# Kernel tuning notes

Hardware: AMD Instinct MI355X
Metric: run time of the kernel (lower is better)

## Reference

```python
import jax, jax.numpy as jnp
import numpy as np

SEQ_LEN, PRED_LEN, ENC_IN, BS = 512, 512, 64, 64


def _main_freq_part(x, k):
    # x: [b, L, c]; rfft over time axis, keep top-k magnitude freqs per (b, c)
    xf = jnp.fft.rfft(x, axis=1)                       # [b, F, c] complex
    mag = jnp.abs(xf)
    _, idx = jax.lax.top_k(jnp.moveaxis(mag, 1, 2), k)  # [b, c, k]
    F = xf.shape[1]
    mask = jax.nn.one_hot(idx, F, dtype=x.dtype).sum(axis=2)  # [b, c, F]
    mask = jnp.moveaxis(mask, 1, 2)                    # [b, F, c]
    x_filt = jnp.fft.irfft(xf * mask, axis=1).astype(jnp.float32)  # n = 2*(F-1) = L (L even)
    return x - x_filt, x_filt


def setup_inputs() -> dict:
    key = jax.random.key(0)
    ks = jax.random.split(key, 16)
    E = ENC_IN
    s = 0.05
    inp = {
        "batch_x": jax.random.normal(ks[0], (BS, SEQ_LEN, ENC_IN), dtype=jnp.float32),
        # nn.MultiheadAttention params (num_heads resolves to 1)
        "in_proj_w": jax.random.normal(ks[1], (3 * E, E), dtype=jnp.float32) * s,
        "in_proj_b": jax.random.normal(ks[2], (3 * E,), dtype=jnp.float32) * s,
        "out_w": jax.random.normal(ks[3], (E, E), dtype=jnp.float32) * s,
        "out_b": jax.random.normal(ks[4], (E,), dtype=jnp.float32) * s,
        # FANLayer params
        "Wp": jax.random.normal(ks[5], (PRED_LEN // 4, SEQ_LEN), dtype=jnp.float32) * s,
        "bp": jax.random.normal(ks[6], (PRED_LEN // 4,), dtype=jnp.float32) * s,
        "Wg": jax.random.normal(ks[7], (PRED_LEN - PRED_LEN // 2, SEQ_LEN), dtype=jnp.float32) * s,
        "bg": jax.random.normal(ks[8], (PRED_LEN - PRED_LEN // 2,), dtype=jnp.float32) * s,
        "gate": jax.random.normal(ks[9], (1,), dtype=jnp.float32),
        # MLP params (input_dim = seq_len + pred_len)
        "fc1_w": jax.random.normal(ks[10], (3 * (SEQ_LEN + PRED_LEN), SEQ_LEN + PRED_LEN), dtype=jnp.float32) * s,
        "fc1_b": jax.random.normal(ks[11], (3 * (SEQ_LEN + PRED_LEN),), dtype=jnp.float32) * s,
        "fc2_w": jax.random.normal(ks[12], (PRED_LEN, 3 * (SEQ_LEN + PRED_LEN)), dtype=jnp.float32) * s,
        "fc2_b": jax.random.normal(ks[13], (PRED_LEN,), dtype=jnp.float32) * s,
        "freq_topk": 20,
    }
    return inp


def reference(batch_x, in_proj_w, in_proj_b, out_w, out_b,
              Wp, bp, Wg, bg, gate, fc1_w, fc1_b, fc2_w, fc2_b, freq_topk):
    E = batch_x.shape[-1]
    norm_input, x_filt = _main_freq_part(batch_x, freq_topk)  # [b, L, c] each

    # --- single-head MultiheadAttention: Q = x_filt, K = V = norm_input ---
    wq, wk, wv = jnp.split(in_proj_w, 3, axis=0)
    bq, bk, bv = jnp.split(in_proj_b, 3, axis=0)
    q = x_filt @ wq.T + bq
    k = norm_input @ wk.T + bk
    v = norm_input @ wv.T + bv
    scores = jnp.einsum('bqe,bke->bqk', q, k) / jnp.sqrt(jnp.asarray(E, batch_x.dtype))
    attn = jax.nn.softmax(scores, axis=-1)
    attn_output = jnp.einsum('bqk,bke->bqe', attn, v) @ out_w.T + out_b  # [b, L, c]

    # --- FANLayer (identical weights per channel -> fully batched) ---
    mf = jnp.swapaxes(x_filt, 1, 2)     # [b, c, L]
    xt = jnp.swapaxes(batch_x, 1, 2)    # [b, c, L]
    g = jax.nn.gelu(mf @ Wg.T + bg, approximate=False)
    p = mf @ Wp.T + bp
    gt = jax.nn.sigmoid(gate)           # (1,) broadcasts
    fan = jnp.concatenate([gt * jnp.cos(p), gt * jnp.sin(p), (1.0 - gt) * g], axis=-1)  # [b, c, pred]
    h = jnp.concatenate([fan, xt], axis=-1)          # [b, c, L + pred]
    mlp = jax.nn.relu(h @ fc1_w.T + fc1_b) @ fc2_w.T + fc2_b  # [b, c, pred]
    pred_main = jnp.swapaxes(mlp, 1, 2)              # [b, pred, c]

    # torch forward('n') returns attn_output and stores pred_main as state;
    # stack both to expose all computed math.
    return jnp.stack([attn_output, pred_main])
```

## Files before the change

kernel.cpp:

```cpp
#include <hip/hip_runtime.h>
#include <math.h>

#define U_HBF   0
#define U_MFT   4194304
#define U_XRE   6291456
#define U_XIM   7344128
#define U_KEEPI 8396800
#define U_KEEPW 8527872
#define U_XFILT 8658944
#define U_NORM  10756096
#define U_Q     6291456
#define U_K     12853248
#define U_V     14950400
#define U_HIDBF 8388608
#define U_W1BF  14680064
#define U_W2BF  16252928
#define U_PART  8658944

#define TWO_PI_OVER_512 0.012271846303085129

typedef __attribute__((ext_vector_type(8))) short short8;
typedef __attribute__((ext_vector_type(4))) float floatx4;

__device__ inline unsigned short f2bf(float f) {
    union { unsigned int i; float f; } x; x.f = f;
    unsigned int r = x.i + 0x7fff + ((x.i >> 16) & 1);
    return (unsigned short)(r >> 16);
}

__global__ __launch_bounds__(256) void dft_split(const float* __restrict__ x,
                                                 float* __restrict__ xre,
                                                 float* __restrict__ xim,
                                                 float* __restrict__ part) {
    __shared__ float xs[64 * 64];
    __shared__ float ct[512], st[512];
    int tid = threadIdx.x;
    int b = blockIdx.y;
    int f0 = blockIdx.x * 64;
    int z = blockIdx.z;
    for (int i = tid; i < 512; i += 256) {
        float s, c; sincosf((float)((double)i * TWO_PI_OVER_512), &s, &c);
        ct[i] = c; st[i] = s;
    }
    int c2 = (tid & 31) * 2;
    int fg = tid >> 5;
    int fb = f0 + fg * 8;
    float2 ar[8], ai[8];
    #pragma unroll
    for (int i = 0; i < 8; ++i) { ar[i] = make_float2(0.f, 0.f); ai[i] = make_float2(0.f, 0.f); }
    for (int sub = 0; sub < 2; ++sub) {
        int t0 = z * 128 + sub * 64;
        __syncthreads();
        for (int i = tid; i < 4096; i += 256)
            xs[i] = x[(size_t)(b * 512 + t0) * 64 + i];
        __syncthreads();
        for (int tt = 0; tt < 64; ++tt) {
            float2 xv = *(float2*)&xs[tt * 64 + c2];
            int t = t0 + tt;
            int idx = (fb * t) & 511;
            #pragma unroll
            for (int i = 0; i < 8; ++i) {
                float cv = ct[idx], sv = st[idx];
                ar[i].x += xv.x * cv; ar[i].y += xv.y * cv;
                ai[i].x -= xv.x * sv; ai[i].y -= xv.y * sv;
                idx = (idx + t) & 511;
            }
        }
    }
    float* dre = (z == 0) ? xre : (part + (size_t)(z - 1) * 2105344);
    float* dim_ = (z == 0) ? xim : (part + (size_t)(z - 1) * 2105344 + 1052672);
    #pragma unroll
    for (int i = 0; i < 8; ++i) {
        int f = fb + i;
        if (f < 257) {
            *(float2*)&dre[((size_t)(b * 257) + f) * 64 + c2] = ar[i];
            *(float2*)&dim_[((size_t)(b * 257) + f) * 64 + c2] = ai[i];
        }
    }
}

__global__ __launch_bounds__(256) void dft_reduce(float* __restrict__ xreflat,
                                                  const float* __restrict__ part) {
    int i = blockIdx.x * 256 + threadIdx.x;
    if (i < 526336) {
        float4 a  = *(float4*)&xreflat[(size_t)i * 4];
        float4 p0 = *(const float4*)&part[(size_t)i * 4];
        float4 p1 = *(const float4*)&part[2105344 + (size_t)i * 4];
        float4 p2 = *(const float4*)&part[4210688 + (size_t)i * 4];
        a.x += p0.x + p1.x + p2.x;
        a.y += p0.y + p1.y + p2.y;
        a.z += p0.z + p1.z + p2.z;
        a.w += p0.w + p1.w + p2.w;
        *(float4*)&xreflat[(size_t)i * 4] = a;
    }
}

__global__ __launch_bounds__(256) void topk_lds(const float* __restrict__ xre,
                                                const float* __restrict__ xim,
                                                int* __restrict__ keepi,
                                                float* __restrict__ keepw,
                                                const int* __restrict__ kptr) {
    __shared__ float vals[320];
    __shared__ float tv[256];
    __shared__ int   ti[256];
    int tid = threadIdx.x;
    int bc = blockIdx.x;
    int b = bc >> 6, c = bc & 63;
    int kk = *kptr; if (kk > 32) kk = 32;
    for (int f = tid; f < 320; f += 256) {
        if (f < 257) {
            size_t a = ((size_t)(b * 257) + f) * 64 + c;
            float re = xre[a], im = xim[a];
            vals[f] = sqrtf(re * re + im * im);
        } else vals[f] = -1.f;
    }
    __syncthreads();
    for (int j = 0; j < kk; ++j) {
        float v0 = vals[tid];
        int   i0 = tid;
        if (tid < 64) {
            float v1 = vals[tid + 256];
            if (v1 > v0) { v0 = v1; i0 = tid + 256; }
        }
        tv[tid] = v0; ti[tid] = i0;
        __syncthreads();
        for (int s = 128; s > 0; s >>= 1) {
            if (tid < s) {
                float ov = tv[tid + s]; int oi = ti[tid + s];
                if (ov > tv[tid] || (ov == tv[tid] && oi < ti[tid])) { tv[tid] = ov; ti[tid] = oi; }
            }
            __syncthreads();
        }
        if (tid == 0) {
            int bf = ti[0];
            keepi[bc * 32 + j] = bf;
            keepw[bc * 32 + j] = (bf == 0 || bf == 256) ? (1.f / 512.f) : (2.f / 512.f);
            vals[bf] = -1.f;
        }
        __syncthreads();
    }
}

__global__ __launch_bounds__(256) void xfilt_fused(const float* __restrict__ x,
                                                   const float* __restrict__ xre,
                                                   const float* __restrict__ xim,
                                                   const int* __restrict__ keepi,
                                                   const float* __restrict__ keepw,
                                                   float* __restrict__ xfilt,
                                                   float* __restrict__ norm,
                                                   float* __restrict__ mft,
                                                   unsigned short* __restrict__ hbf,
                                                   const int* __restrict__ kptr) {
    __shared__ float ct[512], st[512];
    __shared__ int   kf[64 * 33];
    __shared__ float kre[64 * 33], kim[64 * 33];
    __shared__ float xs[64 * 65];
    __shared__ float ft[64 * 65];
    int tid = threadIdx.x;
    int b = blockIdx.y;
    int t0 = blockIdx.x * 64;
    int kk = *kptr; if (kk > 32) kk = 32;
    for (int i = tid; i < 512; i += 256) {
        float s, c; sincosf((float)((double)i * TWO_PI_OVER_512), &s, &c);
        ct[i] = c; st[i] = s;
    }
    for (int i = tid; i < 4096; i += 256) {
        int tl = i >> 6, c = i & 63;
        xs[tl * 65 + c] = x[((size_t)(b * 512) + t0 + tl) * 64 + c];
    }
    for (int e = tid; e < 64 * kk; e += 256) {
        int c = e / kk, j = e - c * kk;
        int bc = b * 64 + c;
        int f = keepi[bc * 32 + j];
        float w = keepw[bc * 32 + j];
        size_t a = ((size_t)(b * 257) + f) * 64 + c;
        kf[c * 33 + j]  = f;
        kre[c * 33 + j] = w * xre[a];
        kim[c * 33 + j] = w * xim[a];
    }
    __syncthreads();
    int l = tid & 63, w = tid >> 6;
    int t = t0 + l;
    for (int ci = 0; ci < 16; ++ci) {
        int c = w * 16 + ci;
        float acc = 0.f;
        for (int j = 0; j < kk; ++j) {
            int f = kf[c * 33 + j];
            int idx = (f * t) & 511;
            acc += kre[c * 33 + j] * ct[idx] - kim[c * 33 + j] * st[idx];
        }
        ft[c * 65 + l] = acc;
    }
    __syncthreads();
    for (int i = tid; i < 4096; i += 256) {
        int tl = i >> 6, c = i & 63;
        float v = ft[c * 65 + tl];
        size_t a = ((size_t)(b * 512) + t0 + tl) * 64 + c;
        xfilt[a] = v;
        norm[a]  = xs[tl * 65 + c] - v;
    }
    for (int i = tid; i < 4096; i += 256) {
        int cr = i >> 6, tl = i & 63;
        mft[((size_t)(b * 64) + cr) * 512 + t0 + tl] = ft[cr * 65 + tl];
        hbf[((size_t)(b * 64) + cr) * 1024 + 512 + t0 + tl] = f2bf(xs[tl * 65 + cr]);
    }
}

__global__ __launch_bounds__(256) void qkv_gemm(const float* __restrict__ xfilt,
                                                const float* __restrict__ norm,
                                                const float* __restrict__ w,
                                                const float* __restrict__ bias,
                                                unsigned short* __restrict__ q,
                                                unsigned short* __restrict__ kmat,
                                                unsigned short* __restrict__ vt) {
    __shared__ float As[32 * 64];
    __shared__ float Bs[32 * 64];
    __shared__ unsigned short Cs[64 * 65];
    int tid = threadIdx.x;
    int tx = tid & 15, ty = tid >> 4;
    int grp = blockIdx.x;
    int m0 = blockIdx.y * 64;
    int n0 = grp * 64;
    const float* A = (grp == 0) ? xfilt : norm;
    float acc[4][4] = {};
    for (int k0 = 0; k0 < 64; k0 += 32) {
        __syncthreads();
        #pragma unroll
        for (int s = 0; s < 2; ++s) {
            int i4 = tid + s * 256;
            int row = i4 >> 3, kq = i4 & 7;
            float4 a4 = *(const float4*)&A[(size_t)(m0 + row) * 64 + k0 + kq * 4];
            float4 w4 = *(const float4*)&w[(size_t)(n0 + row) * 64 + k0 + kq * 4];
            int kb = kq * 4;
            As[(kb + 0) * 64 + row] = a4.x; As[(kb + 1) * 64 + row] = a4.y;
            As[(kb + 2) * 64 + row] = a4.z; As[(kb + 3) * 64 + row] = a4.w;
            Bs[(kb + 0) * 64 + row] = w4.x; Bs[(kb + 1) * 64 + row] = w4.y;
            Bs[(kb + 2) * 64 + row] = w4.z; Bs[(kb + 3) * 64 + row] = w4.w;
        }
        __syncthreads();
        #pragma unroll
        for (int kk = 0; kk < 32; ++kk) {
            float4 a4 = *(const float4*)&As[kk * 64 + (ty << 2)];
            float4 b4 = *(const float4*)&Bs[kk * 64 + (tx << 2)];
            #pragma unroll
            for (int i = 0; i < 4; ++i)
                #pragma unroll
                for (int j = 0; j < 4; ++j)
                    acc[i][j] += (&a4.x)[i] * (&b4.x)[j];
        }
    }
    int row0 = ty * 4, col0 = tx * 4;
    float4 bb = *(const float4*)&bias[n0 + col0];
    #pragma unroll
    for (int i = 0; i < 4; ++i) {
        float v0 = acc[i][0] + bb.x, v1 = acc[i][1] + bb.y;
        float v2 = acc[i][2] + bb.z, v3 = acc[i][3] + bb.w;
        ushort4 o;
        o.x = f2bf(v0); o.y = f2bf(v1); o.z = f2bf(v2); o.w = f2bf(v3);
        if (grp == 0) {
            *(ushort4*)&q[(size_t)(m0 + row0 + i) * 64 + col0] = o;
        } else if (grp == 1) {
            *(ushort4*)&kmat[(size_t)(m0 + row0 + i) * 64 + col0] = o;
        } else {
            Cs[(row0 + i) * 65 + col0 + 0] = o.x;
            Cs[(row0 + i) * 65 + col0 + 1] = o.y;
            Cs[(row0 + i) * 65 + col0 + 2] = o.z;
            Cs[(row0 + i) * 65 + col0 + 3] = o.w;
        }
    }
    if (grp == 2) {
        __syncthreads();
        int b = m0 >> 9, t0 = m0 & 511;
        for (int i2 = tid; i2 < 4096; i2 += 256) {
            int e = i2 >> 6, tl = i2 & 63;
            vt[((size_t)(b * 64) + e) * 512 + t0 + tl] = Cs[tl * 65 + e];
        }
    }
}

__global__ __launch_bounds__(256) void attn_mfma(const unsigned short* __restrict__ qbf,
                                                 const unsigned short* __restrict__ kbf,
                                                 const unsigned short* __restrict__ vtbf,
                                                 const float* __restrict__ ow,
                                                 const float* __restrict__ ob,
                                                 float* __restrict__ out) {
    __shared__ unsigned short Qs[64 * 72];
    __shared__ unsigned short KVs[64 * 72];
    __shared__ unsigned short Pp[4 * 16 * 72];
    int tid = threadIdx.x;
    int l = tid & 63, w = tid >> 6;
    int q = l >> 4, cl = l & 15;
    int b = blockIdx.y, i0 = blockIdx.x * 64;

    for (int i = tid; i < 1024; i += 256) {
        int r = i >> 4, e4 = (i & 15) * 4;
        *(ushort4*)&Qs[r * 72 + e4] = *(const ushort4*)&qbf[((size_t)(b * 512) + i0 + r) * 64 + e4];
    }
    __syncthreads();
    short8 aq0 = *(short8*)&Qs[(w * 16 + cl) * 72 + q * 8];
    short8 aq1 = *(short8*)&Qs[(w * 16 + cl) * 72 + 32 + q * 8];

    floatx4 s[32];
    #pragma unroll
    for (int f = 0; f < 32; ++f) s[f] = (floatx4){0.f, 0.f, 0.f, 0.f};

    #pragma unroll
    for (int ch = 0; ch < 8; ++ch) {
        __syncthreads();
        for (int i = tid; i < 1024; i += 256) {
            int jj = i >> 4, e4 = (i & 15) * 4;
            *(ushort4*)&KVs[jj * 72 + e4] =
                *(const ushort4*)&kbf[((size_t)(b * 512) + ch * 64 + jj) * 64 + e4];
        }
        __syncthreads();
        #pragma unroll
        for (int jt = 0; jt < 4; ++jt) {
            short8 b0 = *(short8*)&KVs[(jt * 16 + cl) * 72 + q * 8];
            short8 b1 = *(short8*)&KVs[(jt * 16 + cl) * 72 + 32 + q * 8];
            s[ch * 4 + jt] = __builtin_amdgcn_mfma_f32_16x16x32_bf16(aq0, b0, s[ch * 4 + jt], 0, 0, 0);
            s[ch * 4 + jt] = __builtin_amdgcn_mfma_f32_16x16x32_bf16(aq1, b1, s[ch * 4 + jt], 0, 0, 0);
        }
    }

    float invl[4];
    #pragma unroll
    for (int r = 0; r < 4; ++r) {
        float m = -1e30f;
        #pragma unroll
        for (int f = 0; f < 32; ++f) m = fmaxf(m, s[f][r]);
        m = fmaxf(m, __shfl_xor(m, 1)); m = fmaxf(m, __shfl_xor(m, 2));
        m = fmaxf(m, __shfl_xor(m, 4)); m = fmaxf(m, __shfl_xor(m, 8));
        float sum = 0.f;
        #pragma unroll
        for (int f = 0; f < 32; ++f) {
            float p = expf((s[f][r] - m) * 0.125f);
            s[f][r] = p; sum += p;
        }
        sum += __shfl_xor(sum, 1); sum += __shfl_xor(sum, 2);
        sum += __shfl_xor(sum, 4); sum += __shfl_xor(sum, 8);
        invl[r] = 1.f / sum;
    }

    floatx4 o4[4];
    #pragma unroll
    for (int nt = 0; nt < 4; ++nt) o4[nt] = (floatx4){0.f, 0.f, 0.f, 0.f};
    #pragma unroll
    for (int ch = 0; ch < 8; ++ch) {
        #pragma unroll
        for (int jt = 0; jt < 4; ++jt)
            #pragma unroll
            for (int r = 0; r < 4; ++r)
                Pp[w * 1152 + (q * 4 + r) * 72 + jt * 16 + cl] = f2bf(s[ch * 4 + jt][r]);
        __syncthreads();
        for (int i = tid; i < 1024; i += 256) {
            int e = i >> 4, j4 = (i & 15) * 4;
            *(ushort4*)&KVs[e * 72 + j4] =
                *(const ushort4*)&vtbf[((size_t)(b * 64) + e) * 512 + ch * 64 + j4];
        }
        __syncthreads();
        #pragma unroll
        for (int ks = 0; ks < 2; ++ks) {
            short8 ap = *(short8*)&Pp[w * 1152 + cl * 72 + ks * 32 + q * 8];
            #pragma unroll
            for (int nt = 0; nt < 4; ++nt) {
                short8 bv = *(short8*)&KVs[(nt * 16 + cl) * 72 + ks * 32 + q * 8];
                o4[nt] = __builtin_amdgcn_mfma_f32_16x16x32_bf16(ap, bv, o4[nt], 0, 0, 0);
            }
        }
    }

    #pragma unroll
    for (int nt = 0; nt < 4; ++nt)
        #pragma unroll
        for (int r = 0; r < 4; ++r)
            Qs[(w * 16 + q * 4 + r) * 72 + nt * 16 + cl] = f2bf(o4[nt][r] * invl[r]);
    __syncthreads();
    for (int i = tid; i < 1024; i += 256) {
        int o = i >> 4, e4 = (i & 15) * 4;
        float4 v = *(const float4*)&ow[o * 64 + e4];
        ushort4 u; u.x = f2bf(v.x); u.y = f2bf(v.y); u.z = f2bf(v.z); u.w = f2bf(v.w);
        *(ushort4*)&KVs[o * 72 + e4] = u;
    }
    __syncthreads();
    floatx4 acc2[4];
    #pragma unroll
    for (int nt = 0; nt < 4; ++nt) acc2[nt] = (floatx4){0.f, 0.f, 0.f, 0.f};
    #pragma unroll
    for (int ks = 0; ks < 2; ++ks) {
        short8 ao = *(short8*)&Qs[(w * 16 + cl) * 72 + ks * 32 + q * 8];
        #pragma unroll
        for (int nt = 0; nt < 4; ++nt) {
            short8 bo = *(short8*)&KVs[(nt * 16 + cl) * 72 + ks * 32 + q * 8];
            acc2[nt] = __builtin_amdgcn_mfma_f32_16x16x32_bf16(ao, bo, acc2[nt], 0, 0, 0);
        }
    }
    #pragma unroll
    for (int nt = 0; nt < 4; ++nt) {
        float bb = ob[nt * 16 + cl];
        #pragma unroll
        for (int r = 0; r < 4; ++r)
            out[((size_t)(b * 512) + i0 + w * 16 + q * 4 + r) * 64 + nt * 16 + cl] = acc2[nt][r] + bb;
    }
}

template<int EPI>
__global__ __launch_bounds__(256) void gemm_k(const float* __restrict__ A,
                                              const float* __restrict__ W,
                                              const float* __restrict__ bias,
                                              unsigned short* __restrict__ C,
                                              int K,
                                              const float* __restrict__ gate) {
    __shared__ float As[32 * 64];
    __shared__ float Bs[32 * 64];
    int tid = threadIdx.x;
    int tx = tid & 15, ty = tid >> 4;
    int m0 = blockIdx.y * 64, n0 = blockIdx.x * 64;
    float acc[4][4] = {};
    for (int k0 = 0; k0 < K; k0 += 32) {
        __syncthreads();
        #pragma unroll
        for (int s = 0; s < 2; ++s) {
            int i4 = tid + s * 256;
            int row = i4 >> 3, kq = i4 & 7;
            float4 a4 = *(const float4*)&A[(size_t)(m0 + row) * K + k0 + kq * 4];
            float4 w4 = *(const float4*)&W[(size_t)(n0 + row) * K + k0 + kq * 4];
            int kb = kq * 4;
            As[(kb + 0) * 64 + row] = a4.x; As[(kb + 1) * 64 + row] = a4.y;
            As[(kb + 2) * 64 + row] = a4.z; As[(kb + 3) * 64 + row] = a4.w;
            Bs[(kb + 0) * 64 + row] = w4.x; Bs[(kb + 1) * 64 + row] = w4.y;
            Bs[(kb + 2) * 64 + row] = w4.z; Bs[(kb + 3) * 64 + row] = w4.w;
        }
        __syncthreads();
        #pragma unroll
        for (int kk = 0; kk < 32; ++kk) {
            float4 a4 = *(const float4*)&As[kk * 64 + (ty << 2)];
            float4 b4 = *(const float4*)&Bs[kk * 64 + (tx << 2)];
            #pragma unroll
            for (int i = 0; i < 4; ++i)
                #pragma unroll
                for (int j = 0; j < 4; ++j)
                    acc[i][j] += (&a4.x)[i] * (&b4.x)[j];
        }
    }
    int row0 = m0 + ty * 4, col0 = n0 + tx * 4;
    float4 bb = *(const float4*)&bias[col0];
    float gt = 1.f / (1.f + expf(-gate[0]));
    #pragma unroll
    for (int i = 0; i < 4; ++i) {
        int row = row0 + i;
        float v0 = acc[i][0] + bb.x, v1 = acc[i][1] + bb.y;
        float v2 = acc[i][2] + bb.z, v3 = acc[i][3] + bb.w;
        if (EPI == 2) {
            ushort4 co, si;
            co.x = f2bf(gt * cosf(v0)); co.y = f2bf(gt * cosf(v1));
            co.z = f2bf(gt * cosf(v2)); co.w = f2bf(gt * cosf(v3));
            si.x = f2bf(gt * sinf(v0)); si.y = f2bf(gt * sinf(v1));
            si.z = f2bf(gt * sinf(v2)); si.w = f2bf(gt * sinf(v3));
            *(ushort4*)&C[(size_t)row * 1024 + col0] = co;
            *(ushort4*)&C[(size_t)row * 1024 + 128 + col0] = si;
        } else if (EPI == 3) {
            float ig = 1.f - gt;
            ushort4 o;
            o.x = f2bf(ig * 0.5f * v0 * (1.f + erff(v0 * 0.70710678118f)));
            o.y = f2bf(ig * 0.5f * v1 * (1.f + erff(v1 * 0.70710678118f)));
            o.z = f2bf(ig * 0.5f * v2 * (1.f + erff(v2 * 0.70710678118f)));
            o.w = f2bf(ig * 0.5f * v3 * (1.f + erff(v3 * 0.70710678118f)));
            *(ushort4*)&C[(size_t)row * 1024 + 256 + col0] = o;
        }
    }
}

__global__ __launch_bounds__(256) void cast_bf16(const float* __restrict__ in,
                                                 unsigned short* __restrict__ out, int n4) {
    int i = blockIdx.x * 256 + threadIdx.x;
    if (i < n4) {
        float4 v = *(const float4*)&in[(size_t)i * 4];
        ushort4 o;
        o.x = f2bf(v.x); o.y = f2bf(v.y); o.z = f2bf(v.z); o.w = f2bf(v.w);
        *(ushort4*)&out[(size_t)i * 4] = o;
    }
}

template<int EPI>
__global__ __launch_bounds__(256) void gemm_mfma(const unsigned short* __restrict__ A,
                                                 const unsigned short* __restrict__ B,
                                                 const float* __restrict__ bias,
                                                 void* __restrict__ Cout,
                                                 int M, int N, int K) {
    __shared__ unsigned short As[8192];
    __shared__ unsigned short Bs[8192];
    int tid = threadIdx.x;
    int l = tid & 63, w = tid >> 6;
    int q = l >> 4, cl = l & 15;
    int wm = w >> 1, wn = w & 1;
    int m0 = blockIdx.y * 128, n0 = blockIdx.x * 128;
    floatx4 acc[4][4];
    #pragma unroll
    for (int i = 0; i < 4; ++i)
        #pragma unroll
        for (int j = 0; j < 4; ++j)
            acc[i][j] = (floatx4){0.f, 0.f, 0.f, 0.f};

    for (int k0 = 0; k0 < K; k0 += 64) {
        __syncthreads();
        #pragma unroll
        for (int ci = 0; ci < 8; ++ci) {
            int cid = w * 8 + ci;
            int isB = cid >> 4;
            int c = cid & 15;
            int cq = c >> 3, cks = (c >> 2) & 1, cf = c & 3;
            int row = cq * 64 + cf * 16 + cl;
            int col = k0 + cks * 32 + q * 8;
            const unsigned short* gp = isB ? (B + (size_t)(n0 + row) * K + col)
                                           : (A + (size_t)(m0 + row) * K + col);
            unsigned short* lp = (isB ? Bs : As) + c * 512;
            __builtin_amdgcn_global_load_lds((const __attribute__((address_space(1))) void*)gp,
                                             (__attribute__((address_space(3))) void*)lp,
                                             16, 0, 0);
        }
        __syncthreads();
        #pragma unroll
        for (int ks = 0; ks < 2; ++ks) {
            short8 af[4], bg[4];
            #pragma unroll
            for (int f = 0; f < 4; ++f) {
                af[f] = *(short8*)&As[(wm * 8 + ks * 4 + f) * 512 + l * 8];
                bg[f] = *(short8*)&Bs[(wn * 8 + ks * 4 + f) * 512 + l * 8];
            }
            #pragma unroll
            for (int i = 0; i < 4; ++i)
                #pragma unroll
                for (int j = 0; j < 4; ++j)
                    acc[i][j] = __builtin_amdgcn_mfma_f32_16x16x32_bf16(af[i], bg[j], acc[i][j], 0, 0, 0);
        }
    }

    if (EPI == 1) {
        unsigned short* Cb = (unsigned short*)Cout;
        #pragma unroll
        for (int j = 0; j < 4; ++j) {
            int col = n0 + wn * 64 + j * 16 + cl;
            float bb = bias[col];
            #pragma unroll
            for (int i = 0; i < 4; ++i) {
                int rowb = m0 + wm * 64 + i * 16 + q * 4;
                #pragma unroll
                for (int r = 0; r < 4; ++r) {
                    float v = acc[i][j][r] + bb;
                    Cb[(size_t)(rowb + r) * N + col] = f2bf(fmaxf(v, 0.f));
                }
            }
        }
    } else {
        float* Ob = (float*)Cout;
        int bidx = (n0 >> 6) + wn;
        #pragma unroll
        for (int i = 0; i < 4; ++i) {
            #pragma unroll
            for (int r = 0; r < 4; ++r) {
                int t = m0 + wm * 64 + i * 16 + q * 4 + r;
                float bb = bias[t];
                #pragma unroll
                for (int j = 0; j < 4; ++j) {
                    int c = j * 16 + cl;
                    Ob[((size_t)bidx * 512 + t) * 64 + c] = acc[i][j][r] + bb;
                }
            }
        }
    }
}

extern "C" void kernel_launch(void* const* d_in, const int* in_sizes, int n_in,
                              void* d_out, int out_size, void* d_ws, size_t ws_size,
                              hipStream_t stream) {
    const float* x         = (const float*)d_in[0];
    const float* in_proj_w = (const float*)d_in[1];
    const float* in_proj_b = (const float*)d_in[2];
    const float* out_w     = (const float*)d_in[3];
    const float* out_b     = (const float*)d_in[4];
    const float* Wp        = (const float*)d_in[5];
    const float* bp        = (const float*)d_in[6];
    const float* Wg        = (const float*)d_in[7];
    const float* bg        = (const float*)d_in[8];
    const float* gate      = (const float*)d_in[9];
    const float* fc1_w     = (const float*)d_in[10];
    const float* fc1_b     = (const float*)d_in[11];
    const float* fc2_w     = (const float*)d_in[12];
    const float* fc2_b     = (const float*)d_in[13];
    const int*   kptr      = (const int*)d_in[14];
    float* ws  = (float*)d_ws;
    float* out = (float*)d_out;

    float* mft   = ws + U_MFT;
    float* xre   = ws + U_XRE;
    float* xim   = ws + U_XIM;
    int*   keepi = (int*)(ws + U_KEEPI);
    float* keepw = ws + U_KEEPW;
    float* xfilt = ws + U_XFILT;
    float* norm  = ws + U_NORM;
    float* part  = ws + U_PART;
    unsigned short* hbf   = (unsigned short*)(ws + U_HBF);
    unsigned short* qb    = (unsigned short*)(ws + U_Q);
    unsigned short* kb    = (unsigned short*)(ws + U_K);
    unsigned short* vtb   = (unsigned short*)(ws + U_V);
    unsigned short* hidbf = (unsigned short*)(ws + U_HIDBF);
    unsigned short* w1bf  = (unsigned short*)(ws + U_W1BF);
    unsigned short* w2bf  = (unsigned short*)(ws + U_W2BF);

    dft_split  <<<dim3(5, 64, 4), 256, 0, stream>>>(x, xre, xim, part);
    dft_reduce <<<dim3(2056),     256, 0, stream>>>(xre, part);
    topk_lds   <<<dim3(4096),     256, 0, stream>>>(xre, xim, keepi, keepw, kptr);
    xfilt_fused<<<dim3(8, 64),    256, 0, stream>>>(x, xre, xim, keepi, keepw, xfilt, norm, mft, hbf, kptr);
    qkv_gemm   <<<dim3(3, 512),   256, 0, stream>>>(xfilt, norm, in_proj_w, in_proj_b, qb, kb, vtb);
    attn_mfma  <<<dim3(8, 64),    256, 0, stream>>>(qb, kb, vtb, out_w, out_b, out);
    gemm_k<2>  <<<dim3(2, 64),    256, 0, stream>>>(mft, Wp, bp, hbf, 512, gate);
    gemm_k<3>  <<<dim3(4, 64),    256, 0, stream>>>(mft, Wg, bg, hbf, 512, gate);
    cast_bf16<<<3072, 256, 0, stream>>>(fc1_w, w1bf, 786432);
    cast_bf16<<<1536, 256, 0, stream>>>(fc2_w, w2bf, 393216);
    gemm_mfma<1><<<dim3(24, 32), 256, 0, stream>>>(hbf,  w1bf,  fc1_b, hidbf,         4096, 3072, 1024);
    gemm_mfma<2><<<dim3(32, 4),  256, 0, stream>>>(w2bf, hidbf, fc2_b, out + 2097152, 512,  4096, 3072);
}
```

Measured before the change: 617.8 us.

## Split-K the fc2 MFMA GEMM into four partial sums plus a reduce kernel

The fc2 GEMM (M=512, N=4096, K=3072) previously ran on only 128 workgroups, which underfills a 256-CU device, and each workgroup walked a long K loop. It is now split along K into four 768-wide chunks across a z grid dimension, giving 512 workgroups. Each chunk writes fp32 partials into workspace reused from the dead hbf/mft region. A new elementwise kernel sums the four partials and adds the bias. The trade-off is about 64 MB of extra partial-sum traffic and one more kernel launch.

```diff
diff --git a/kernel.cpp b/kernel.cpp
--- a/kernel.cpp
+++ b/kernel.cpp
@@ -2,6 +2,7 @@
 #include <math.h>
 
 #define U_HBF   0
+#define U_FC2P  0
 #define U_MFT   4194304
 #define U_XRE   6291456
 #define U_XIM   7344128
@@ -481,12 +482,11 @@
     }
 }
 
-template<int EPI>
-__global__ __launch_bounds__(256) void gemm_mfma(const unsigned short* __restrict__ A,
-                                                 const unsigned short* __restrict__ B,
-                                                 const float* __restrict__ bias,
-                                                 void* __restrict__ Cout,
-                                                 int M, int N, int K) {
+__global__ __launch_bounds__(256) void gemm_mfma1(const unsigned short* __restrict__ A,
+                                                  const unsigned short* __restrict__ B,
+                                                  const float* __restrict__ bias,
+                                                  unsigned short* __restrict__ Cb,
+                                                  int M, int N, int K) {
     __shared__ unsigned short As[8192];
     __shared__ unsigned short Bs[8192];
     int tid = threadIdx.x;
@@ -535,38 +535,109 @@
         }
     }
 
-    if (EPI == 1) {
-        unsigned short* Cb = (unsigned short*)Cout;
-        #pragma unroll
-        for (int j = 0; j < 4; ++j) {
-            int col = n0 + wn * 64 + j * 16 + cl;
-            float bb = bias[col];
-            #pragma unroll
-            for (int i = 0; i < 4; ++i) {
-                int rowb = m0 + wm * 64 + i * 16 + q * 4;
+    #pragma unroll
+    for (int j = 0; j < 4; ++j) {
+        int col = n0 + wn * 64 + j * 16 + cl;
+        float bb = bias[col];
+        #pragma unroll
+        for (int i = 0; i < 4; ++i) {
+            int rowb = m0 + wm * 64 + i * 16 + q * 4;
+            #pragma unroll
+            for (int r = 0; r < 4; ++r) {
+                float v = acc[i][j][r] + bb;
+                Cb[(size_t)(rowb + r) * N + col] = f2bf(fmaxf(v, 0.f));
+            }
+        }
+    }
+}
+
+__global__ __launch_bounds__(256) void gemm_fc2_split(const unsigned short* __restrict__ A,
+                                                      const unsigned short* __restrict__ B,
+                                                      float* __restrict__ part,
+                                                      int K) {
+    __shared__ unsigned short As[8192];
+    __shared__ unsigned short Bs[8192];
+    int tid = threadIdx.x;
+    int l = tid & 63, w = tid >> 6;
+    int q = l >> 4, cl = l & 15;
+    int wm = w >> 1, wn = w & 1;
+    int m0 = blockIdx.y * 128, n0 = blockIdx.x * 128;
+    int kbeg = blockIdx.z * 768;
+    floatx4 acc[4][4];
+    #pragma unroll
+    for (int i = 0; i < 4; ++i)
+        #pragma unroll
+        for (int j = 0; j < 4; ++j)
+            acc[i][j] = (floatx4){0.f, 0.f, 0.f, 0.f};
+
+    for (int k0 = kbeg; k0 < kbeg + 768; k0 += 64) {
+        __syncthreads();
+        #pragma unroll
+        for (int ci = 0; ci < 8; ++ci) {
+            int cid = w * 8 + ci;
+            int isB = cid >> 4;
+            int c = cid & 15;
+            int cq = c >> 3, cks = (c >> 2) & 1, cf = c & 3;
+            int row = cq * 64 + cf * 16 + cl;
+            int col = k0 + cks * 32 + q * 8;
+            const unsigned short* gp = isB ? (B + (size_t)(n0 + row) * K + col)
+                                           : (A + (size_t)(m0 + row) * K + col);
+            unsigned short* lp = (isB ? Bs : As) + c * 512;
+            __builtin_amdgcn_global_load_lds((const __attribute__((address_space(1))) void*)gp,
+                                             (__attribute__((address_space(3))) void*)lp,
+                                             16, 0, 0);
+        }
+        __syncthreads();
+        #pragma unroll
+        for (int ks = 0; ks < 2; ++ks) {
+            short8 af[4], bg[4];
+            #pragma unroll
+            for (int f = 0; f < 4; ++f) {
+                af[f] = *(short8*)&As[(wm * 8 + ks * 4 + f) * 512 + l * 8];
+                bg[f] = *(short8*)&Bs[(wn * 8 + ks * 4 + f) * 512 + l * 8];
+            }
+            #pragma unroll
+            for (int i = 0; i < 4; ++i)
                 #pragma unroll
-                for (int r = 0; r < 4; ++r) {
-                    float v = acc[i][j][r] + bb;
-                    Cb[(size_t)(rowb + r) * N + col] = f2bf(fmaxf(v, 0.f));
-                }
+                for (int j = 0; j < 4; ++j)
+                    acc[i][j] = __builtin_amdgcn_mfma_f32_16x16x32_bf16(af[i], bg[j], acc[i][j], 0, 0, 0);
+        }
+    }
+
+    float* Ob = part + (size_t)blockIdx.z * 2097152;
+    int bidx = (n0 >> 6) + wn;
+    #pragma unroll
+    for (int i = 0; i < 4; ++i) {
+        #pragma unroll
+        for (int r = 0; r < 4; ++r) {
+            int t = m0 + wm * 64 + i * 16 + q * 4 + r;
+            #pragma unroll
+            for (int j = 0; j < 4; ++j) {
+                int c = j * 16 + cl;
+                Ob[((size_t)bidx * 512 + t) * 64 + c] = acc[i][j][r];
             }
         }
-    } else {
-        float* Ob = (float*)Cout;
-        int bidx = (n0 >> 6) + wn;
-        #pragma unroll
-        for (int i = 0; i < 4; ++i) {
-            #pragma unroll
-            for (int r = 0; r < 4; ++r) {
-                int t = m0 + wm * 64 + i * 16 + q * 4 + r;
-                float bb = bias[t];
-                #pragma unroll
-                for (int j = 0; j < 4; ++j) {
-                    int c = j * 16 + cl;
-                    Ob[((size_t)bidx * 512 + t) * 64 + c] = acc[i][j][r] + bb;
-                }
-            }
-        }
+    }
+}
+
+__global__ __launch_bounds__(256) void fc2_reduce(const float* __restrict__ part,
+                                                  const float* __restrict__ bias,
+                                                  float* __restrict__ out) {
+    int i = blockIdx.x * 256 + threadIdx.x;
+    if (i < 524288) {
+        size_t e = (size_t)i * 4;
+        int t = (int)((e >> 6) & 511);
+        float bb = bias[t];
+        float4 p0 = *(const float4*)&part[e];
+        float4 p1 = *(const float4*)&part[2097152 + e];
+        float4 p2 = *(const float4*)&part[4194304 + e];
+        float4 p3 = *(const float4*)&part[6291456 + e];
+        float4 o;
+        o.x = p0.x + p1.x + p2.x + p3.x + bb;
+        o.y = p0.y + p1.y + p2.y + p3.y + bb;
+        o.z = p0.z + p1.z + p2.z + p3.z + bb;
+        o.w = p0.w + p1.w + p2.w + p3.w + bb;
+        *(float4*)&out[e] = o;
     }
 }
 
@@ -599,6 +670,7 @@
     float* xfilt = ws + U_XFILT;
     float* norm  = ws + U_NORM;
     float* part  = ws + U_PART;
+    float* fc2p  = ws + U_FC2P;
     unsigned short* hbf   = (unsigned short*)(ws + U_HBF);
     unsigned short* qb    = (unsigned short*)(ws + U_Q);
     unsigned short* kb    = (unsigned short*)(ws + U_K);
@@ -617,6 +689,7 @@
     gemm_k<3>  <<<dim3(4, 64),    256, 0, stream>>>(mft, Wg, bg, hbf, 512, gate);
     cast_bf16<<<3072, 256, 0, stream>>>(fc1_w, w1bf, 786432);
     cast_bf16<<<1536, 256, 0, stream>>>(fc2_w, w2bf, 393216);
-    gemm_mfma<1><<<dim3(24, 32), 256, 0, stream>>>(hbf,  w1bf,  fc1_b, hidbf,         4096, 3072, 1024);
-    gemm_mfma<2><<<dim3(32, 4),  256, 0, stream>>>(w2bf, hidbf, fc2_b, out + 2097152, 512,  4096, 3072);
-}
+    gemm_mfma1    <<<dim3(24, 32),   256, 0, stream>>>(hbf, w1bf, fc1_b, hidbf, 4096, 3072, 1024);
+    gemm_fc2_split<<<dim3(32, 4, 4), 256, 0, stream>>>(w2bf, hidbf, fc2p, 3072);
+    fc2_reduce    <<<dim3(2048),     256, 0, stream>>>(fc2p, fc2_b, out + 2097152);
+}
```

After: 495.9 us, median of 2. 19.7% less time.
